# Kernel optimization log

Measured on AMD Instinct MI355X. Metric: run time of the kernel, lower is better.

Reference implementation:

```python
import jax, jax.numpy as jnp
import numpy as np

WINDOWS = [1, 3, 5]
LN_EPS = 1e-5
N, C, H, W = 16, 64, 160, 160


def conv1x1(x, w, b):
    # x: [N,C,H,W], w: [O,C], b: [O]  (1x1 conv == channel matmul)
    return jnp.einsum('nchw,oc->nohw', x, w) + b[None, :, None, None]


def _patch_idx(H_, W_, kh, kw, sh, sw):
    nh = (H_ - kh) // sh + 1
    nw = (W_ - kw) // sw + 1
    hi = jnp.arange(nh)[:, None] * sh + jnp.arange(kh)[None, :]  # [nh,kh]
    wi = jnp.arange(nw)[:, None] * sw + jnp.arange(kw)[None, :]  # [nw,kw]
    return nh, nw, hi, wi


def unfold(x, kh, kw, sh, sw):
    # matches torch.nn.functional.unfold: out [N, C*kh*kw, nh*nw]
    n, c, H_, W_ = x.shape
    nh, nw, hi, wi = _patch_idx(H_, W_, kh, kw, sh, sw)
    p = x[:, :, hi[:, None, :, None], wi[None, :, None, :]]      # [N,C,nh,nw,kh,kw]
    p = jnp.transpose(p, (0, 1, 4, 5, 2, 3))                      # [N,C,kh,kw,nh,nw]
    return p.reshape(n, c * kh * kw, nh * nw)


def fold(u, H_, W_, kh, kw, sh, sw):
    # matches torch.nn.functional.fold (overlap add)
    n = u.shape[0]
    nh, nw, hi, wi = _patch_idx(H_, W_, kh, kw, sh, sw)
    c = u.shape[1] // (kh * kw)
    p = u.reshape(n, c, kh, kw, nh, nw)
    p = jnp.transpose(p, (0, 1, 4, 5, 2, 3))                      # [N,C,nh,nw,kh,kw]
    out = jnp.zeros((n, c, H_, W_), u.dtype)
    return out.at[:, :, hi[:, None, :, None], wi[None, :, None, :]].add(p)


def psa(x, ch_wv_w, ch_wv_b, ch_wq_w, ch_wq_b, ch_wz_w, ch_wz_b,
        ln_g, ln_b, sp_wv_w, sp_wv_b, sp_wq_w, sp_wq_b):
    # Polarized Self-Attention (parallel): channel-only + spatial-only branches
    b, c, h, w = x.shape
    hw = h * w
    c2 = c // 2
    # channel-only branch
    wv = conv1x1(x, ch_wv_w, ch_wv_b).reshape(b, c2, hw)
    wq = jax.nn.softmax(conv1x1(x, ch_wq_w, ch_wq_b).reshape(b, hw), axis=-1)
    wz = jnp.einsum('bch,bh->bc', wv, wq)                         # [b,c2]
    z = jnp.einsum('bc,oc->bo', wz, ch_wz_w) + ch_wz_b            # [b,c]
    mu = jnp.mean(z, axis=-1, keepdims=True)
    var = jnp.var(z, axis=-1, keepdims=True)
    zn = (z - mu) * jax.lax.rsqrt(var + LN_EPS) * ln_g + ln_b     # LayerNorm(c)
    ch_out = jax.nn.sigmoid(zn)[:, :, None, None] * x
    # spatial-only branch
    swv = conv1x1(x, sp_wv_w, sp_wv_b).reshape(b, c2, hw)
    swq = jax.nn.softmax(jnp.mean(conv1x1(x, sp_wq_w, sp_wq_b), axis=(2, 3)), axis=-1)
    smap = jax.nn.sigmoid(jnp.einsum('bc,bch->bh', swq, swv)).reshape(b, 1, h, w)
    return ch_out + smap * x


def setup_inputs() -> dict:
    key = jax.random.key(0)
    ks = jax.random.split(key, 12)
    c, c2, nw_ = C, C // 2, len(WINDOWS)
    s = 0.05
    return {
        'x': jax.random.normal(ks[0], (N, C, H, W), jnp.float32),
        'exp_w': jax.random.normal(ks[1], (nw_ * c, c), jnp.float32) * s,
        'exp_b': jnp.zeros((nw_ * c,), jnp.float32),
        'res_w': jax.random.normal(ks[2], (c, nw_ * c), jnp.float32) * s,
        'res_b': jnp.zeros((c,), jnp.float32),
        'fus_w': jax.random.normal(ks[3], (c, c), jnp.float32) * s,
        'fus_b': jnp.zeros((c,), jnp.float32),
        'ch_wv_w': jax.random.normal(ks[4], (c2, c), jnp.float32) * s,
        'ch_wv_b': jnp.zeros((c2,), jnp.float32),
        'ch_wq_w': jax.random.normal(ks[5], (1, c), jnp.float32) * s,
        'ch_wq_b': jnp.zeros((1,), jnp.float32),
        'ch_wz_w': jax.random.normal(ks[6], (c, c2), jnp.float32) * s,
        'ch_wz_b': jnp.zeros((c,), jnp.float32),
        'ln_g': jnp.ones((c,), jnp.float32),
        'ln_b': jnp.zeros((c,), jnp.float32),
        'sp_wv_w': jax.random.normal(ks[7], (c2, c), jnp.float32) * s,
        'sp_wv_b': jnp.zeros((c2,), jnp.float32),
        'sp_wq_w': jax.random.normal(ks[8], (c2, c), jnp.float32) * s,
        'sp_wq_b': jnp.zeros((c2,), jnp.float32),
    }


def reference(x, exp_w, exp_b, res_w, res_b, fus_w, fus_b,
              ch_wv_w, ch_wv_b, ch_wq_w, ch_wq_b, ch_wz_w, ch_wz_b,
              ln_g, ln_b, sp_wv_w, sp_wv_b, sp_wq_w, sp_wq_b):
    n, c, h, w = x.shape
    psa_params = (ch_wv_w, ch_wv_b, ch_wq_w, ch_wq_b, ch_wz_w, ch_wz_b,
                  ln_g, ln_b, sp_wv_w, sp_wv_b, sp_wq_w, sp_wq_b)
    ex = conv1x1(x, exp_w, exp_b)                                 # [N, 3C, H, W]
    chunks = jnp.split(ex, len(WINDOWS), axis=1)
    outs = []
    for i, win in enumerate(WINDOWS):
        sh, sw = h // win, w // win
        kh, kw = sh + h % win, sw + w % win
        u = unfold(chunks[i], kh, kw, sh, sw)
        # faithful to torch source: raw view (no permute) into patch images
        a = psa(u.reshape(-1, c, kh, kw), *psa_params)
        a = a.reshape(n, c * kh * kw, win * win)
        cnt = fold(jnp.ones_like(a), h, w, kh, kw, sh, sw)        # overlap counts
        outs.append(fold(a, h, w, kh, kw, sh, sw) / cnt)
    cat = jnp.concatenate(outs, axis=1) + ex
    return conv1x1(conv1x1(cat, res_w, res_b) + x, fus_w, fus_b)
```

## Files before the change

### kernel.cpp

```cpp
#include <hip/hip_runtime.h>
#include <hip/hip_bf16.h>

typedef __hip_bfloat16 bf16;
typedef __attribute__((ext_vector_type(4))) unsigned int u32x4;
typedef __attribute__((ext_vector_type(4))) float f32x4;
typedef __attribute__((ext_vector_type(8))) short bf16x8;
#define DEV __device__ __forceinline__


constexpr int FO_Q     = 0;
constexpr int FO_SMAP  = 1239104;
constexpr int FO_XM    = 2478208;
constexpr int FO_T     = 2514048;
constexpr int FO_SIGA  = 2549888;
constexpr int FO_G     = 2585728;
constexpr int FO_BM    = 2621568;
constexpr int FO_BINV  = 2622128;
constexpr int FO_GB    = 2622688;
constexpr int FO_EXPT  = 2623248;
constexpr int FO_EXPB  = 2635536;
constexpr int FO_WBIGT = 2635728;
constexpr int FO_BCOMB = 2652112;
constexpr int FO_WFRAG = 2652176;
constexpr int FB_SIZE  = 2660368;

__device__ unsigned short g_ex_u[78643200];
__device__ unsigned short g_ex2_u[104857600];
__device__ float          g_fb[FB_SIZE];

template<int WIN> struct WP;
template<> struct WP<1> { static constexpr int WI=0, SH=160, KH=160, K=25600, P=1,  B=16,  QOFF=0,      BOFF=0;   };
template<> struct WP<3> { static constexpr int WI=1, SH=53,  KH=54,  K=2916,  P=9,  B=144, QOFF=409600, BOFF=16;  };
template<> struct WP<5> { static constexpr int WI=2, SH=32,  KH=32,  K=1024,  P=25, B=400, QOFF=829504, BOFF=160; };

template<int WIN> DEV void decomp(int f, int& c, int& kidx, int& p) {
  constexpr int P = WP<WIN>::P, K = WP<WIN>::K;
  int m;
  if constexpr (P == 1) { p = 0; m = f; }
  else { m = f / P; p = f - m * P; }
  c = m / K; kidx = m - c * K;
}

template<int WIN> DEV void stepK(int& c, int& kidx, int& p) {
  constexpr int K = WP<WIN>::K, P = WP<WIN>::P;
  if constexpr (P == 1) { kidx += K; }
  else {
    constexpr int KMP = K % P, KDP = K / P;
    if constexpr (KMP == 0) { kidx += KDP; }
    else { p += KMP; if (p >= P) { p -= P; kidx += KDP + 1; } else kidx += KDP; }
  }
  if (kidx >= K) { kidx -= K; ++c; }
}

template<int WIN> DEV int pix(int kidx, int p) {
  constexpr int KH = WP<WIN>::KH, SH = WP<WIN>::SH;
  if constexpr (WIN == 1) return kidx;
  int ki = kidx / KH, kj = kidx - ki * KH;
  int ph = p / WIN,  pw = p - ph * WIN;
  return (ph * SH + ki) * 160 + pw * SH + kj;
}

DEV unsigned short bfbits(float f) {
  bf16 b = __float2bfloat16(f);
  unsigned short u;
  __builtin_memcpy(&u, &b, 2);
  return u;
}

DEV float bf2f(unsigned short u) {
  bf16 b;
  __builtin_memcpy(&b, &u, 2);
  return __bfloat162float(b);
}

DEV void store8bf(bf16* p, const unsigned short* ob) {
  u32x4 v = { (unsigned)ob[0] | ((unsigned)ob[1] << 16),
              (unsigned)ob[2] | ((unsigned)ob[3] << 16),
              (unsigned)ob[4] | ((unsigned)ob[5] << 16),
              (unsigned)ob[6] | ((unsigned)ob[7] << 16) };
  *(u32x4*)p = v;
}

DEV bf16x8 as_bf16x8(u32x4 v) {
  union { u32x4 u; bf16x8 b; } x; x.u = v; return x.b;
}

DEV void wave_reduce64_atomic(float* dst, float (&part)[64], int lane) {
#pragma unroll
  for (int s = 0; s < 6; ++s) {
    const int m = 1 << s, half = 32 >> s;
#pragma unroll
    for (int i = 0; i < half; ++i) {
      float lo = part[i], hi = part[i + half];
      float keep = (lane & m) ? hi : lo;
      float sv   = (lane & m) ? lo : hi;
      float recv = __shfl_xor(sv, m, 64);
      part[i] = keep + recv;
    }
  }
  int chn = (int)(__brev((unsigned)lane) >> 26);
  atomicAdd(dst + chn, part[0]);
}

__global__ __launch_bounds__(256)
void k_prep(const float* __restrict__ exp_w, const float* __restrict__ exp_b,
            const float* __restrict__ res_w, const float* __restrict__ res_b,
            const float* __restrict__ fus_w, const float* __restrict__ fus_b) {
  float* fb = g_fb;
  int gt = blockIdx.x * 256 + threadIdx.x;
  if (gt < 12288) {
    int oc = gt % 192, f = gt / 192;
    float a = 0.f;
    for (int o = 0; o < 64; ++o)
      a += fus_w[f*64+o] * res_w[o*192+oc];
    fb[FO_WBIGT + oc*64 + f] = a;
  } else if (gt < 16384) {
    int t2 = gt - 12288; int o = t2 % 64, f = t2 / 64;
    fb[FO_WBIGT + (192+o)*64 + f] = fus_w[f*64+o];
  } else if (gt < 16448) {
    int f = gt - 16384;
    float a = fus_b[f];
    for (int o = 0; o < 64; ++o)
      a += fus_w[f*64+o] * res_b[o];
    fb[FO_BCOMB + f] = a;
  } else if (gt < 28736) {
    int t3 = gt - 16448; int o = t3 % 192, c = t3 / 192;
    fb[FO_EXPT + c*192 + o] = exp_w[o*64+c];
  } else if (gt < 28928) {
    int o = gt - 28736;
    fb[FO_EXPB + o] = exp_b[o];
  } else if (gt < 28928 + 71680) {
    fb[FO_XM + gt - 28928] = 0.f;
  }
}

__global__ __launch_bounds__(256)
void k_prep2() {
  float* fb = g_fb;
  bf16* wf = (bf16*)(fb + FO_WFRAG);
  int t = blockIdx.x * 256 + threadIdx.x;
  int j  = t & 7;
  int l  = (t >> 3) & 63;
  int ks = (t >> 9) & 7;
  int wv = t >> 12;
  int k = ks*32 + (l >> 4)*8 + j;
  int o = wv*16 + (l & 15);
  wf[t] = __float2bfloat16(fb[FO_WBIGT + k*64 + o]);
}

__global__ __launch_bounds__(256)
void k_ex(const float* __restrict__ x) {
  const float* fb = g_fb;
  bf16* ex  = (bf16*)g_ex_u;
  bf16* ex2 = (bf16*)g_ex2_u;
  __shared__ float xs[64*64];
  int blk = blockIdx.x; int n = blk / 400; int s0 = (blk % 400) * 64;
  int tid = threadIdx.x;
  for (int e = tid; e < 4096; e += 256) {
    int c = e >> 6, px = e & 63;
    xs[e] = x[(n*64 + c)*25600 + s0 + px];
  }
  __syncthreads();
  int px = tid & 63;
  int rg = tid >> 6;
  bf16* e2row = ex2 + (size_t)(n*25600 + s0 + px)*256;
  unsigned short ob[8];
  if (rg == 3) {
#pragma unroll
    for (int r = 0; r < 8; ++r) {
#pragma unroll
      for (int i = 0; i < 8; ++i)
        ob[i] = bfbits(xs[(r*8 + i)*64 + px]);
      store8bf(e2row + 192 + r*8, ob);
    }
    return;
  }
  int o0 = __builtin_amdgcn_readfirstlane(rg * 64);
  float acc[64];
#pragma unroll
  for (int j = 0; j < 64; ++j) acc[j] = fb[FO_EXPB + o0 + j];
  const float* wT = fb + FO_EXPT;
  for (int c = 0; c < 64; ++c) {
    float xv = xs[(c << 6) + px];
    const float* wr = wT + c*192 + o0;
#pragma unroll
    for (int j = 0; j < 64; ++j) acc[j] += wr[j] * xv;
  }
  bf16* eo = ex + (size_t)(n*192 + o0)*25600 + s0 + px;
#pragma unroll
  for (int j = 0; j < 64; ++j) eo[(size_t)j*25600] = __float2bfloat16(acc[j]);
#pragma unroll
  for (int r = 0; r < 8; ++r) {
#pragma unroll
    for (int i = 0; i < 8; ++i)
      ob[i] = bfbits(acc[r*8 + i]);
    store8bf(e2row + o0 + r*8, ob);
  }
}

template<int WIN, int CH, int CHUNK, int ITERS>
DEV void p1_body(int idx, const float* __restrict__ chq_w, float wqb) {
  using W = WP<WIN>;
  constexpr int K = W::K, P = W::P, CK = 64*K, WI = W::WI, QOFF = W::QOFF,
                BOFF = W::BOFF;
  float* fb = g_fb;
  const bf16* ex  = (const bf16*)g_ex_u;
  const bf16* ex2 = (const bf16*)g_ex2_u;
  int bi = idx / CH, ch = idx - bi*CH;
  int n = bi / P, bl = bi - n*P; int bg = BOFF + bi;
  int base = ch*CHUNK;
  int send = (base + CHUNK < K) ? base + CHUNK : K;
  const bf16* exn = ex + (size_t)(n*192 + WI*64)*25600;
  float* qout = fb + FO_Q + QOFF + (size_t)bi*K;
  int tid = threadIdx.x, lane = tid & 63;
  float wq[64];
#pragma unroll
  for (int j = 0; j < 64; ++j) wq[j] = chq_w[j];
  float part[64];
#pragma unroll
  for (int j = 0; j < 64; ++j) part[j] = 0.f;
  for (int it = 0; it < ITERS; ++it) {
    int sp = base + it*256 + tid;
    if (sp < send) {
      float dot = 0.f;
      if constexpr (WIN == 1) {
        const u32x4* e2 = (const u32x4*)(ex2 + (size_t)(n*25600 + sp)*256);
#pragma unroll
        for (int r = 0; r < 8; ++r) {
          u32x4 v = e2[r];
#pragma unroll
          for (int i = 0; i < 4; ++i) {
            int c = r*8 + 2*i;
            float lo = bf2f((unsigned short)(v[i] & 0xffffu));
            float hi = bf2f((unsigned short)(v[i] >> 16));
            part[c]   += lo;  dot += wq[c]   * lo;
            part[c+1] += hi;  dot += wq[c+1] * hi;
          }
        }
      } else {
        int f = bl*CK + sp;
        int c, kidx, p; decomp<WIN>(f, c, kidx, p);
#pragma unroll
        for (int j = 0; j < 64; ++j) {
          float v = __bfloat162float(exn[c*25600 + pix<WIN>(kidx, p)]);
          part[j] += v;
          dot += wq[j] * v;
          stepK<WIN>(c, kidx, p);
        }
      }
      qout[sp] = dot + wqb;
    }
  }
  wave_reduce64_atomic(fb + FO_XM + bg*64, part, lane);
}

__global__ __launch_bounds__(256, 2)
void k_p1all(const float* __restrict__ chq_w, const float* __restrict__ chq_b) {
  float wqb = chq_b[0];
  int blk = blockIdx.x;
  if (blk < 400)      p1_body<1,25,1024,4>(blk,       chq_w, wqb);
  else if (blk < 832) p1_body<3, 3, 972,4>(blk - 400, chq_w, wqb);
  else                p1_body<5, 2, 512,2>(blk - 832, chq_w, wqb);
}

__global__ __launch_bounds__(256)
void k_bstats(const float* __restrict__ spq_w, const float* __restrict__ spq_b,
              const float* __restrict__ spv_w, const float* __restrict__ spv_b) {
  float* fb = g_fb;
  __shared__ float red[256]; __shared__ float sqs[32]; __shared__ float swq[32];
  int bg = blockIdx.x, tid = threadIdx.x;
  int Kk, qo, bi;
  if (bg < 16)       { Kk = 25600; qo = 0;      bi = bg;       }
  else if (bg < 160) { Kk = 2916;  qo = 409600; bi = bg - 16;  }
  else               { Kk = 1024;  qo = 829504; bi = bg - 160; }
  const float* lg = fb + FO_Q + qo + (size_t)bi*Kk;
  float m = -1e30f;
  for (int s = tid; s < Kk; s += 256) m = fmaxf(m, lg[s]);
  red[tid] = m; __syncthreads();
  for (int st = 128; st; st >>= 1) { if (tid < st) red[tid] = fmaxf(red[tid], red[tid+st]); __syncthreads(); }
  float M = red[0]; __syncthreads();
  float ss = 0.f;
  for (int s = tid; s < Kk; s += 256) ss += __expf(lg[s] - M);
  red[tid] = ss; __syncthreads();
  for (int st = 128; st; st >>= 1) { if (tid < st) red[tid] += red[tid+st]; __syncthreads(); }
  if (tid == 0) { fb[FO_BM + bg] = M; fb[FO_BINV + bg] = 1.f / red[0]; }
  const float* xm_b = fb + FO_XM + bg*64;
  float rK = 1.f / (float)Kk;
  if (tid < 32) {
    float a = spq_b[tid];
    for (int c = 0; c < 64; ++c)
      a += spq_w[tid*64 + c] * (xm_b[c] * rK);
    sqs[tid] = a;
  }
  __syncthreads();
  if (tid == 0) {
    float mx = -1e30f;
    for (int o = 0; o < 32; ++o) mx = fmaxf(mx, sqs[o]);
    float z = 0.f;
    for (int o = 0; o < 32; ++o) { float e = __expf(sqs[o] - mx); swq[o] = e; z += e; }
    float rz = 1.f / z;
    for (int o = 0; o < 32; ++o) swq[o] *= rz;
  }
  __syncthreads();
  if (tid < 64) {
    float a = 0.f;
    for (int o = 0; o < 32; ++o) a += swq[o] * spv_w[o*64 + tid];
    fb[FO_G + bg*64 + tid] = a;
  }
  if (tid == 64) {
    float gb = 0.f;
    for (int o = 0; o < 32; ++o) gb += swq[o] * spv_b[o];
    fb[FO_GB + bg] = gb;
  }
}

template<int WIN, int CH, int CHUNK, int ITERS>
DEV void p2_body(int idx) {
  using W = WP<WIN>;
  constexpr int K = W::K, P = W::P, CK = 64*K, WI = W::WI, QOFF = W::QOFF,
                BOFF = W::BOFF;
  float* fb = g_fb;
  const bf16* ex  = (const bf16*)g_ex_u;
  const bf16* ex2 = (const bf16*)g_ex2_u;
  int bi = idx / CH, ch = idx - bi*CH;
  int n = bi / P, bl = bi - n*P; int bg = BOFF + bi;
  int base = ch*CHUNK;
  int send = (base + CHUNK < K) ? base + CHUNK : K;
  const bf16* exn = ex + (size_t)(n*192 + WI*64)*25600;
  const float* qin = fb + FO_Q + QOFF + (size_t)bi*K;
  float* so = fb + FO_SMAP + QOFF + (size_t)bi*K;
  float M = fb[FO_BM + bg], inv = fb[FO_BINV + bg];
  float gbs = fb[FO_GB + bg];
  int tid = threadIdx.x, lane = tid & 63;
  float gs[64];
#pragma unroll
  for (int j = 0; j < 64; ++j) gs[j] = fb[FO_G + bg*64 + j];
  float part[64];
#pragma unroll
  for (int j = 0; j < 64; ++j) part[j] = 0.f;
  for (int it = 0; it < ITERS; ++it) {
    int sp = base + it*256 + tid;
    if (sp < send) {
      float qv = __expf(qin[sp] - M) * inv;
      float dot = 0.f;
      if constexpr (WIN == 1) {
        const u32x4* e2 = (const u32x4*)(ex2 + (size_t)(n*25600 + sp)*256);
#pragma unroll
        for (int r = 0; r < 8; ++r) {
          u32x4 v = e2[r];
#pragma unroll
          for (int i = 0; i < 4; ++i) {
            int c = r*8 + 2*i;
            float lo = bf2f((unsigned short)(v[i] & 0xffffu));
            float hi = bf2f((unsigned short)(v[i] >> 16));
            part[c]   += qv * lo;  dot += gs[c]   * lo;
            part[c+1] += qv * hi;  dot += gs[c+1] * hi;
          }
        }
      } else {
        int f = bl*CK + sp;
        int c, kidx, p; decomp<WIN>(f, c, kidx, p);
#pragma unroll
        for (int j = 0; j < 64; ++j) {
          float v = __bfloat162float(exn[c*25600 + pix<WIN>(kidx, p)]);
          part[j] += qv * v;
          dot += gs[j] * v;
          stepK<WIN>(c, kidx, p);
        }
      }
      so[sp] = 1.f / (1.f + __expf(-(dot + gbs)));
    }
  }
  wave_reduce64_atomic(fb + FO_T + bg*64, part, lane);
}

__global__ __launch_bounds__(256, 2)
void k_p2all() {
  int blk = blockIdx.x;
  if (blk < 400)      p2_body<1,25,1024,4>(blk);
  else if (blk < 832) p2_body<3, 3, 972,4>(blk - 400);
  else                p2_body<5, 2, 512,2>(blk - 832);
}

__global__ __launch_bounds__(64)
void k_zln(const float* __restrict__ chv_w, const float* __restrict__ chv_b,
           const float* __restrict__ chz_w, const float* __restrict__ chz_b,
           const float* __restrict__ ln_g,  const float* __restrict__ ln_b) {
  float* fb = g_fb;
  __shared__ float wzs[32]; __shared__ float zsh[64]; __shared__ float mom[2];
  int bg = blockIdx.x, tid = threadIdx.x;
  const float* t_b = fb + FO_T + bg*64;
  if (tid < 32) {
    float a = chv_b[tid];
    for (int c = 0; c < 64; ++c)
      a += chv_w[tid*64 + c] * t_b[c];
    wzs[tid] = a;
  }
  __syncthreads();
  float zv = chz_b[tid];
  for (int o = 0; o < 32; ++o)
    zv += chz_w[tid*32 + o] * wzs[o];
  zsh[tid] = zv;
  __syncthreads();
  if (tid == 0) {
    float mu = 0.f;
    for (int j = 0; j < 64; ++j) mu += zsh[j];
    mu *= (1.f/64.f);
    float m2 = 0.f;
    for (int j = 0; j < 64; ++j) { float d = zsh[j] - mu; m2 += d*d; }
    m2 *= (1.f/64.f);
    mom[0] = mu; mom[1] = rsqrtf(m2 + 1e-5f);
  }
  __syncthreads();
  float zn = (zv - mom[0]) * mom[1] * ln_g[tid] + ln_b[tid];
  fb[FO_SIGA + bg*64 + tid] = 1.f / (1.f + __expf(-zn));
}

template<int WIN> DEV void gate_rows3(int n, int s, int h, int w, int px,
                                      const float* __restrict__ fb,
                                      const bf16* __restrict__ e2row,
                                      bf16* extT) {
  using W = WP<WIN>;
  constexpr int SH = W::SH, KH = W::KH, K = W::K, P = W::P, WI = W::WI,
                QOFF = W::QOFF, BOFF = W::BOFF;
  const float* smap = fb + FO_SMAP + QOFF + (size_t)(n*P)*K;
  const float* sg   = fb + FO_SIGA + (size_t)(BOFF + n*P)*64;
  const u32x4* src = (const u32x4*)(e2row + WI*64);
  u32x4 vv[8];
#pragma unroll
  for (int r = 0; r < 8; ++r) vv[r] = src[r];
  int swz = (px & 7) << 3;
  unsigned short ob[8];
  if constexpr (WIN == 1) {
    float sm = smap[s];
#pragma unroll
    for (int r = 0; r < 8; ++r) {
#pragma unroll
      for (int i = 0; i < 4; ++i) {
        int c = r*8 + 2*i;
        float lo = bf2f((unsigned short)(vv[r][i] & 0xffffu));
        float hi = bf2f((unsigned short)(vv[r][i] >> 16));
        ob[2*i]   = bfbits(lo * (1.f + sg[c]   + sm));
        ob[2*i+1] = bfbits(hi * (1.f + sg[c+1] + sm));
      }
      store8bf(&extT[px*256 + ((WI*64 + r*8) ^ swz)], ob);
    }
  } else {
    int phmin = (h >= KH) ? (h - KH)/SH + 1 : 0;
    int phmax = (WIN-1 < h/SH) ? WIN-1 : h/SH;
    int pwmin = (w >= KH) ? (w - KH)/SH + 1 : 0;
    int pwmax = (WIN-1 < w/SH) ? WIN-1 : w/SH;
    int cf[4]; int s0s[4]; int np = 0;
    for (int ph = phmin; ph <= phmax; ++ph)
      for (int pw = pwmin; pw <= pwmax; ++pw) {
        int ki = h - ph*SH, kj = w - pw*SH;
        unsigned base0 = (unsigned)((ki*KH + kj)*P + ph*WIN + pw);
        unsigned q = base0 / (unsigned)K;
        cf[np] = (int)q; s0s[np] = (int)(base0 - q*(unsigned)K); ++np;
      }
    float rc = 1.f / (float)np;
    int hi4[4]; float smv[4];
#pragma unroll
    for (int t = 0; t < 4; ++t)
      if (t < np) { hi4[t] = cf[t] >> 6; smv[t] = smap[hi4[t]*K + s0s[t]]; }
#pragma unroll
    for (int r = 0; r < 8; ++r) {
#pragma unroll
      for (int cc = 0; cc < 8; ++cc) {
        float gsum = 0.f;
#pragma unroll
        for (int t = 0; t < 4; ++t) {
          if (t < np) {
            int v = cf[t];
            int h2 = v >> 6;
            if (h2 != hi4[t]) { hi4[t] = h2; smv[t] = smap[h2*K + s0s[t]]; }
            gsum += sg[v] + smv[t];
            cf[t] = v + P;
          }
        }
        unsigned wd = vv[r][cc >> 1];
        unsigned short eb = (cc & 1) ? (unsigned short)(wd >> 16)
                                     : (unsigned short)(wd & 0xffffu);
        ob[cc] = bfbits(bf2f(eb) * (1.f + gsum * rc));
      }
      store8bf(&extT[px*256 + ((WI*64 + r*8) ^ swz)], ob);
    }
  }
}

__global__ __launch_bounds__(256)
void k_final(float* __restrict__ out) {
  const float* fb = g_fb;
  const bf16* ex2 = (const bf16*)g_ex2_u;
  __shared__ __align__(16) bf16 extT[64*256];
  int blk = blockIdx.x; int n = blk / 400; int s0 = (blk % 400) * 64;
  int tid = threadIdx.x;
  int rg = tid >> 6; int px = tid & 63;
  int s = s0 + px; int h = s / 160; int w = s - h*160;
  const bf16* e2row = ex2 + (size_t)(n*25600 + s)*256;
  if (rg == 3) {
    const u32x4* src = (const u32x4*)(e2row + 192);
    int swz = (px & 7) << 3;
#pragma unroll
    for (int r = 0; r < 8; ++r)
      *(u32x4*)&extT[px*256 + ((192 + r*8) ^ swz)] = src[r];
  } else if (rg == 0) gate_rows3<1>(n, s, h, w, px, fb, e2row, extT);
  else if (rg == 1)   gate_rows3<3>(n, s, h, w, px, fb, e2row, extT);
  else                gate_rows3<5>(n, s, h, w, px, fb, e2row, extT);
  __syncthreads();

  int wv = tid >> 6; int l = tid & 63;
  int lx = l & 15, g = l >> 4;
  const u32x4* wfA = (const u32x4*)(fb + FO_WFRAG);
  u32x4 af[8];
#pragma unroll
  for (int ks = 0; ks < 8; ++ks) af[ks] = wfA[(wv*8 + ks)*64 + l];
  f32x4 acc[4];
#pragma unroll
  for (int pt = 0; pt < 4; ++pt) acc[pt] = f32x4{0.f, 0.f, 0.f, 0.f};
#pragma unroll
  for (int ks = 0; ks < 8; ++ks) {
#pragma unroll
    for (int pt = 0; pt < 4; ++pt) {
      int pxx = pt*16 + lx;
      const u32x4* bp = (const u32x4*)&extT[pxx*256 + ((ks*32 + g*8) ^ ((pxx & 7) << 3))];
      acc[pt] = __builtin_amdgcn_mfma_f32_16x16x32_bf16(
                  as_bf16x8(af[ks]), as_bf16x8(*bp), acc[pt], 0, 0, 0);
    }
  }
  float bia[4];
#pragma unroll
  for (int r = 0; r < 4; ++r) bia[r] = fb[FO_BCOMB + wv*16 + g*4 + r];
#pragma unroll
  for (int pt = 0; pt < 4; ++pt) {
#pragma unroll
    for (int r = 0; r < 4; ++r)
      out[(size_t)(n*64 + wv*16 + g*4 + r)*25600 + s0 + pt*16 + lx] = acc[pt][r] + bia[r];
  }
}

extern "C" void kernel_launch(void* const* d_in, const int* in_sizes, int n_in,
                              void* d_out, int out_size, void* d_ws, size_t ws_size,
                              hipStream_t stream) {
  const float* x     = (const float*)d_in[0];
  const float* exp_w = (const float*)d_in[1];
  const float* exp_b = (const float*)d_in[2];
  const float* res_w = (const float*)d_in[3];
  const float* res_b = (const float*)d_in[4];
  const float* fus_w = (const float*)d_in[5];
  const float* fus_b = (const float*)d_in[6];
  const float* chv_w = (const float*)d_in[7];
  const float* chv_b = (const float*)d_in[8];
  const float* chq_w = (const float*)d_in[9];
  const float* chq_b = (const float*)d_in[10];
  const float* chz_w = (const float*)d_in[11];
  const float* chz_b = (const float*)d_in[12];
  const float* ln_g  = (const float*)d_in[13];
  const float* ln_b  = (const float*)d_in[14];
  const float* spv_w = (const float*)d_in[15];
  const float* spv_b = (const float*)d_in[16];
  const float* spq_w = (const float*)d_in[17];
  const float* spq_b = (const float*)d_in[18];
  float* out = (float*)d_out;

  k_prep<<<393, 256, 0, stream>>>(exp_w, exp_b, res_w, res_b, fus_w, fus_b);
  k_prep2<<<64, 256, 0, stream>>>();
  k_ex<<<6400, 256, 0, stream>>>(x);

  k_p1all<<<1632, 256, 0, stream>>>(chq_w, chq_b);

  k_bstats<<<560, 256, 0, stream>>>(spq_w, spq_b, spv_w, spv_b);

  k_p2all<<<1632, 256, 0, stream>>>();

  k_zln<<<560, 64, 0, stream>>>(chv_w, chv_b, chz_w, chz_b, ln_g, ln_b);

  k_final<<<6400, 256, 0, stream>>>(out);
}
```

Baseline: 859.5 us.

## Drop channel-major ex buffer; read windows from pixel-major ex2 layout

Removes the separate channel-major bf16 copy of the expanded activations and has the window-3/5 paths of both attention passes gather from the pixel-major ex2 buffer instead. k_ex is rebalanced so each of the four waves computes 48 output channels and copies 16 input channels, rather than three waves computing 64 while one copies. This removes about 160 MB of global writes and leaves one fewer buffer competing for cache. The cost is that gathers for windows 3 and 5 now stride 512 bytes between pixels, which may reduce coalescing in p1/p2.

```diff
diff --git a/kernel.cpp b/kernel.cpp
--- a/kernel.cpp
+++ b/kernel.cpp
@@ -24,7 +24,6 @@
 constexpr int FO_WFRAG = 2652176;
 constexpr int FB_SIZE  = 2660368;
 
-__device__ unsigned short g_ex_u[78643200];
 __device__ unsigned short g_ex2_u[104857600];
 __device__ float          g_fb[FB_SIZE];
 
@@ -151,7 +150,6 @@
 __global__ __launch_bounds__(256)
 void k_ex(const float* __restrict__ x) {
   const float* fb = g_fb;
-  bf16* ex  = (bf16*)g_ex_u;
   bf16* ex2 = (bf16*)g_ex2_u;
   __shared__ float xs[64*64];
   int blk = blockIdx.x; int n = blk / 400; int s0 = (blk % 400) * 64;
@@ -162,39 +160,32 @@
   }
   __syncthreads();
   int px = tid & 63;
-  int rg = tid >> 6;
+  int wv = tid >> 6;
+  int o0 = __builtin_amdgcn_readfirstlane(wv * 48);
   bf16* e2row = ex2 + (size_t)(n*25600 + s0 + px)*256;
-  unsigned short ob[8];
-  if (rg == 3) {
-#pragma unroll
-    for (int r = 0; r < 8; ++r) {
-#pragma unroll
-      for (int i = 0; i < 8; ++i)
-        ob[i] = bfbits(xs[(r*8 + i)*64 + px]);
-      store8bf(e2row + 192 + r*8, ob);
-    }
-    return;
-  }
-  int o0 = __builtin_amdgcn_readfirstlane(rg * 64);
-  float acc[64];
-#pragma unroll
-  for (int j = 0; j < 64; ++j) acc[j] = fb[FO_EXPB + o0 + j];
+  float acc[48];
+#pragma unroll
+  for (int j = 0; j < 48; ++j) acc[j] = fb[FO_EXPB + o0 + j];
   const float* wT = fb + FO_EXPT;
   for (int c = 0; c < 64; ++c) {
     float xv = xs[(c << 6) + px];
     const float* wr = wT + c*192 + o0;
 #pragma unroll
-    for (int j = 0; j < 64; ++j) acc[j] += wr[j] * xv;
-  }
-  bf16* eo = ex + (size_t)(n*192 + o0)*25600 + s0 + px;
-#pragma unroll
-  for (int j = 0; j < 64; ++j) eo[(size_t)j*25600] = __float2bfloat16(acc[j]);
-#pragma unroll
-  for (int r = 0; r < 8; ++r) {
+    for (int j = 0; j < 48; ++j) acc[j] += wr[j] * xv;
+  }
+  unsigned short ob[8];
+#pragma unroll
+  for (int r = 0; r < 6; ++r) {
+#pragma unroll
+    for (int i = 0; i < 8; ++i) ob[i] = bfbits(acc[r*8 + i]);
+    store8bf(e2row + o0 + r*8, ob);
+  }
+#pragma unroll
+  for (int r = 0; r < 2; ++r) {
 #pragma unroll
     for (int i = 0; i < 8; ++i)
-      ob[i] = bfbits(acc[r*8 + i]);
-    store8bf(e2row + o0 + r*8, ob);
+      ob[i] = bfbits(xs[(wv*16 + r*8 + i)*64 + px]);
+    store8bf(e2row + 192 + wv*16 + r*8, ob);
   }
 }
 
@@ -204,13 +195,12 @@
   constexpr int K = W::K, P = W::P, CK = 64*K, WI = W::WI, QOFF = W::QOFF,
                 BOFF = W::BOFF;
   float* fb = g_fb;
-  const bf16* ex  = (const bf16*)g_ex_u;
   const bf16* ex2 = (const bf16*)g_ex2_u;
   int bi = idx / CH, ch = idx - bi*CH;
   int n = bi / P, bl = bi - n*P; int bg = BOFF + bi;
   int base = ch*CHUNK;
   int send = (base + CHUNK < K) ? base + CHUNK : K;
-  const bf16* exn = ex + (size_t)(n*192 + WI*64)*25600;
+  const bf16* e2n = ex2 + (size_t)n*25600*256 + WI*64;
   float* qout = fb + FO_Q + QOFF + (size_t)bi*K;
   int tid = threadIdx.x, lane = tid & 63;
   float wq[64];
@@ -224,7 +214,7 @@
     if (sp < send) {
       float dot = 0.f;
       if constexpr (WIN == 1) {
-        const u32x4* e2 = (const u32x4*)(ex2 + (size_t)(n*25600 + sp)*256);
+        const u32x4* e2 = (const u32x4*)(e2n + (size_t)sp*256);
 #pragma unroll
         for (int r = 0; r < 8; ++r) {
           u32x4 v = e2[r];
@@ -242,7 +232,7 @@
         int c, kidx, p; decomp<WIN>(f, c, kidx, p);
 #pragma unroll
         for (int j = 0; j < 64; ++j) {
-          float v = __bfloat162float(exn[c*25600 + pix<WIN>(kidx, p)]);
+          float v = bf2f(((const unsigned short*)e2n)[(size_t)pix<WIN>(kidx, p)*256 + c]);
           part[j] += v;
           dot += wq[j] * v;
           stepK<WIN>(c, kidx, p);
@@ -320,13 +310,12 @@
   constexpr int K = W::K, P = W::P, CK = 64*K, WI = W::WI, QOFF = W::QOFF,
                 BOFF = W::BOFF;
   float* fb = g_fb;
-  const bf16* ex  = (const bf16*)g_ex_u;
   const bf16* ex2 = (const bf16*)g_ex2_u;
   int bi = idx / CH, ch = idx - bi*CH;
   int n = bi / P, bl = bi - n*P; int bg = BOFF + bi;
   int base = ch*CHUNK;
   int send = (base + CHUNK < K) ? base + CHUNK : K;
-  const bf16* exn = ex + (size_t)(n*192 + WI*64)*25600;
+  const bf16* e2n = ex2 + (size_t)n*25600*256 + WI*64;
   const float* qin = fb + FO_Q + QOFF + (size_t)bi*K;
   float* so = fb + FO_SMAP + QOFF + (size_t)bi*K;
   float M = fb[FO_BM + bg], inv = fb[FO_BINV + bg];
@@ -344,7 +333,7 @@
       float qv = __expf(qin[sp] - M) * inv;
       float dot = 0.f;
       if constexpr (WIN == 1) {
-        const u32x4* e2 = (const u32x4*)(ex2 + (size_t)(n*25600 + sp)*256);
+        const u32x4* e2 = (const u32x4*)(e2n + (size_t)sp*256);
 #pragma unroll
         for (int r = 0; r < 8; ++r) {
           u32x4 v = e2[r];
@@ -362,7 +351,7 @@
         int c, kidx, p; decomp<WIN>(f, c, kidx, p);
 #pragma unroll
         for (int j = 0; j < 64; ++j) {
-          float v = __bfloat162float(exn[c*25600 + pix<WIN>(kidx, p)]);
+          float v = bf2f(((const unsigned short*)e2n)[(size_t)pix<WIN>(kidx, p)*256 + c]);
           part[j] += qv * v;
           dot += gs[j] * v;
           stepK<WIN>(c, kidx, p);
```

Result: slower. 2.439 ms (+183.8%).
